# Kernel optimization log

Measured on AMD Instinct MI355X. Metric: run time of the kernel, lower is better.

Reference implementation:

```python
import jax, jax.numpy as jnp
import numpy as np

NUM_HEADS = 4


def setup_inputs() -> dict:
    key = jax.random.key(0)
    ks = jax.random.split(key, 5)
    B, S, E = 32, 1024, 512
    T, Q = 128, 256
    src_encodings = jax.random.normal(ks[0], (B, S, E), dtype=jnp.float32)
    src_token_mask = jax.random.randint(ks[1], (B, S), 0, 2).astype(bool)
    query_vec = jax.random.normal(ks[2], (T, B, Q), dtype=jnp.float32)
    # torch Linear weights are (out_features, in_features)
    W_src = jax.random.normal(ks[3], (NUM_HEADS * Q, E), dtype=jnp.float32) * (1.0 / np.sqrt(E))
    W_opt = jax.random.normal(ks[4], (NUM_HEADS, Q), dtype=jnp.float32) * (1.0 / np.sqrt(Q))
    return {"src_encodings": src_encodings, "src_token_mask": src_token_mask,
            "query_vec": query_vec, "W_src": W_src, "W_opt": W_opt}


def reference(src_encodings, src_token_mask, query_vec, W_src, W_opt):
    B, S, _ = src_encodings.shape
    T = query_vec.shape[0]
    Q = query_vec.shape[2]
    # project + leaky_relu (torch default negative_slope=0.01), split into heads
    proj = jax.nn.leaky_relu(jnp.einsum('bse,fe->bsf', src_encodings, W_src))  # (B,S,H*Q)
    proj = proj.reshape(B, S, NUM_HEADS, Q)                                    # (B,S,H,Q)
    # per-head scores: (T,B,S,H)
    weights = jnp.einsum('bshq,tbq->tbsh', proj, query_vec)
    # head routing: argmax over options scores (T,B,H) -> top-1 head per (t,b)
    options_scores = jnp.einsum('tbq,hq->tbh', query_vec, W_opt)
    best = jnp.argmax(options_scores, axis=-1)                                 # (T,B)
    w = jnp.take_along_axis(weights, best[:, :, None, None], axis=-1)[..., 0]  # (T,B,S)
    # mask and softmax over source positions
    w = jnp.where(src_token_mask[None, :, :], -jnp.inf, w)
    return jax.nn.softmax(w, axis=-1)
```

## Files before the change

### kernel.cpp

```cpp
#include <hip/hip_runtime.h>
#include <hip/hip_bf16.h>
#include <math.h>

#define B_ 32
#define S_ 1024
#define E_ 512
#define T_ 128
#define Q_ 256
#define H_ 4
#define F_ (H_ * Q_)
#define M_ (B_ * S_)

typedef _Float16 f16x8 __attribute__((ext_vector_type(8)));
typedef float f32x4 __attribute__((ext_vector_type(4)));
typedef unsigned int uint32;

__device__ __forceinline__ float lrelu(float x) { return x > 0.0f ? x : 0.01f * x; }

__device__ __forceinline__ uint32 packh2(float a, float b) {
    union { _Float16 h[2]; uint32 u; } v;
    v.h[0] = (_Float16)a; v.h[1] = (_Float16)b;
    return v.u;
}
__device__ __forceinline__ unsigned short packh1(float a) {
    union { _Float16 h; unsigned short u; } v;
    v.h = (_Float16)a;
    return v.u;
}

#define GLOAD_LDS16(g, l)                                                       \
    __builtin_amdgcn_global_load_lds(                                           \
        (const __attribute__((address_space(1))) void*)(g),                     \
        (__attribute__((address_space(3))) void*)(l), 16, 0, 0)

#define SRCW_BLOCKS 4096
#define WW_BLOCKS   128
#define HS_BLOCKS   1024

__global__ __launch_bounds__(256) void prep_kernel(
    float* src, float* wsrc,
    const float* __restrict__ qv, const float* __restrict__ Wopt,
    int* __restrict__ best) {
    const int blk = blockIdx.x;
    if (blk < SRCW_BLOCKS + WW_BLOCKS) {
        float* base = (blk < SRCW_BLOCKS) ? src : wsrc;
        const size_t w0 = (size_t)((blk < SRCW_BLOCKS) ? blk : (blk - SRCW_BLOCKS)) * 64;
        const int tid = threadIdx.x;
        const size_t c = w0 + (tid >> 2);
        const int j = tid & 3;
        const float* rp = base + c * 64 + j * 16;
        float4 v0 = ((const float4*)rp)[0];
        float4 v1 = ((const float4*)rp)[1];
        float4 v2 = ((const float4*)rp)[2];
        float4 v3 = ((const float4*)rp)[3];
        uint4 o0 = make_uint4(packh2(v0.x, v0.y), packh2(v0.z, v0.w),
                              packh2(v1.x, v1.y), packh2(v1.z, v1.w));
        uint4 o1 = make_uint4(packh2(v2.x, v2.y), packh2(v2.z, v2.w),
                              packh2(v3.x, v3.y), packh2(v3.z, v3.w));
        char* op = (char*)(base + c * 64) + j * 32;
        ((uint4*)op)[0] = o0;
        ((uint4*)op)[1] = o1;
    } else {
        const int wave = threadIdx.x >> 6, lane = threadIdx.x & 63;
        const int idx = (blk - SRCW_BLOCKS - WW_BLOCKS) * 4 + wave;
        const float4 qq = *(const float4*)(qv + (size_t)idx * Q_ + lane * 4);
        float s[4];
#pragma unroll
        for (int h = 0; h < 4; ++h) {
            float4 w = *(const float4*)(Wopt + h * Q_ + lane * 4);
            s[h] = qq.x * w.x + qq.y * w.y + qq.z * w.z + qq.w * w.w;
        }
#pragma unroll
        for (int off = 32; off >= 1; off >>= 1) {
#pragma unroll
            for (int h = 0; h < 4; ++h) s[h] += __shfl_down(s[h], off);
        }
        if (lane == 0) {
            int bh = 0; float bs = s[0];
            if (s[1] > bs) { bs = s[1]; bh = 1; }
            if (s[2] > bs) { bs = s[2]; bh = 2; }
            if (s[3] > bs) { bs = s[3]; bh = 3; }
            best[idx] = bh;
        }
    }
}

__global__ __launch_bounds__(256, 2) void proj_score_kernel(
    const unsigned char* __restrict__ Apk,
    const unsigned char* __restrict__ Wpk,
    const float* __restrict__ qv,
    const int* __restrict__ best,
    float* __restrict__ bufs)
{
    __shared__ uint4 smem4[4800];
    char* smem = (char*)smem4;

    const int bid = blockIdx.x;
    const int xcd = bid & 7;
    const int q_ = bid >> 3;
    const int bi = xcd * 32 + (q_ >> 2);
    const int bj = q_ & 3;

    const int tid = threadIdx.x;
    const int wave = tid >> 6, lane = tid & 63;
    const int wm = wave >> 1, wn = wave & 1;
    const int quad = lane >> 4;
    const int fr = lane & 15;
    const int xr = fr & 7;

    const size_t Abase = (size_t)(bi * 128) * 2048;
    const size_t Wbase = (size_t)(bj * 256) * 2048;

    const int r16 = lane >> 2;
    const int slot = lane & 3;
    const int sgb = ((slot ^ ((r16 >> 1) & 3)) & 3) * 16;
    const unsigned char* gA = Apk + Abase + (size_t)(wave * 32 + r16) * 2048 + sgb;
    const unsigned char* gW = Wpk + Wbase + (size_t)(wave * 64 + r16) * 2048 + sgb;

    const int koB = ((quad ^ ((fr >> 1) & 3)) & 3) * 16;
    const int aoff = (wm * 64 + fr) * 64 + koB;
    const int boff = (wn * 128 + fr) * 64 + koB;

    f32x4 acc[4][8] = {};

#define STAGE(bufb_, ks_) do {                                                 \
    const int hb_ = ((ks_) >> 1) * 256 + ((ks_) & 1) * 64;                     \
    _Pragma("unroll")                                                          \
    for (int c_ = 0; c_ < 2; ++c_) {                                           \
        GLOAD_LDS16(gA + (size_t)c_ * 16 * 2048 + hb_,                         \
                    smem + (bufb_) + (wave * 2 + c_) * 1024);                  \
    }                                                                          \
    _Pragma("unroll")                                                          \
    for (int c_ = 0; c_ < 4; ++c_) {                                           \
        GLOAD_LDS16(gW + (size_t)c_ * 16 * 2048 + hb_,                         \
                    smem + (bufb_) + 8192 + (wave * 4 + c_) * 1024);           \
    }                                                                          \
} while (0)

    STAGE(0, 0);
    STAGE(24576, 1);
    asm volatile("s_waitcnt vmcnt(6)" ::: "memory");
    __builtin_amdgcn_s_barrier();

    int cur = 0;
#pragma unroll 1
    for (int ks = 0; ks < 16; ++ks) {
        f16x8 ah[4], bh8[8];
#pragma unroll
        for (int i_ = 0; i_ < 4; ++i_)
            ah[i_] = *(const f16x8*)(smem + cur + aoff + i_ * 1024);
#pragma unroll
        for (int j_ = 0; j_ < 8; ++j_)
            bh8[j_] = *(const f16x8*)(smem + cur + 8192 + boff + j_ * 1024);
        asm volatile("s_waitcnt lgkmcnt(0)" ::: "memory");
        __builtin_amdgcn_s_barrier();
        if (ks < 14) STAGE(cur, ks + 2);
        __builtin_amdgcn_s_setprio(1);
#pragma unroll
        for (int i_ = 0; i_ < 4; ++i_)
#pragma unroll
            for (int j_ = 0; j_ < 8; ++j_) {
                acc[i_][j_] = __builtin_amdgcn_mfma_f32_16x16x32_f16(ah[i_], bh8[j_], acc[i_][j_], 0, 0, 0);
            }
        __builtin_amdgcn_s_setprio(0);
        if (ks < 14) {
            asm volatile("s_waitcnt vmcnt(6)" ::: "memory");
        } else if (ks == 14) {
            asm volatile("s_waitcnt vmcnt(0)" ::: "memory");
        }
        if (ks < 15) __builtin_amdgcn_s_barrier();
        cur ^= 24576;
    }

#undef STAGE

    const int b = bi >> 3;
    const int sbase = (bi & 7) * 128;

    __syncthreads();
    int* tl = (int*)(smem + 73728);
    int* lcnt = (int*)(smem + 74240);
    if (tid == 0) *lcnt = 0;
    __syncthreads();
    if (tid < 128) {
        if (best[tid * B_ + b] == bj) {
            int slot2 = atomicAdd(lcnt, 1);
            tl[slot2] = tid;
        }
    }
    __syncthreads();
    const int n = *lcnt;

#pragma unroll
    for (int i = 0; i < 4; ++i) {
#pragma unroll
        for (int j = 0; j < 8; ++j) {
            int col = wn * 128 + j * 16 + fr;
            int g = col >> 3;
            int cb = (col & 7) * 2;
#pragma unroll
            for (int r = 0; r < 4; ++r) {
                int rr = wm * 64 + i * 16 + quad * 4 + r;
                int gs = (g & 24) | ((g ^ rr) & 7);
                *(unsigned short*)(smem + rr * 512 + gs * 16 + cb) =
                    packh1(lrelu(acc[i][j][r]));
            }
        }
    }
    __syncthreads();

    const int t_idx = tid >> 4, seg = tid & 15;

    for (int tc = 0; tc < n; tc += 16) {
        int nn = min(16, n - tc);
        if (t_idx < nn) {
            int tt = tl[tc + t_idx];
            const float* qp = qv + ((size_t)tt * B_ + b) * Q_ + seg * 16;
            float4 f0 = *(const float4*)(qp);
            float4 f1 = *(const float4*)(qp + 4);
            float4 f2 = *(const float4*)(qp + 8);
            float4 f3 = *(const float4*)(qp + 12);
            uint4 h0 = make_uint4(packh2(f0.x, f0.y), packh2(f0.z, f0.w),
                                  packh2(f1.x, f1.y), packh2(f1.z, f1.w));
            uint4 h1 = make_uint4(packh2(f2.x, f2.y), packh2(f2.z, f2.w),
                                  packh2(f3.x, f3.y), packh2(f3.z, f3.w));
            int g0 = seg * 2, g1 = seg * 2 + 1;
            int gs0 = (g0 & 24) | ((g0 ^ t_idx) & 7);
            int gs1 = (g1 & 24) | ((g1 ^ t_idx) & 7);
            *(uint4*)(smem + 65536 + t_idx * 512 + gs0 * 16) = h0;
            *(uint4*)(smem + 65536 + t_idx * 512 + gs1 * 16) = h1;
        }
        __syncthreads();

#pragma unroll
        for (int sub = 0; sub < 2; ++sub) {
            const int sblk = wave * 2 + sub;
            const int srow = sblk * 16 + fr;
            f32x4 sc = {0.f, 0.f, 0.f, 0.f};
#pragma unroll
            for (int ks2 = 0; ks2 < 8; ++ks2) {
                int kb = ks2 * 4 + quad;
                int ko = ((kb & 24) | ((kb ^ xr) & 7)) * 16;
                f16x8 ph = *(const f16x8*)(smem + srow * 512 + ko);
                f16x8 qh = *(const f16x8*)(smem + 65536 + fr * 512 + ko);
                sc = __builtin_amdgcn_mfma_f32_16x16x32_f16(qh, ph, sc, 0, 0, 0);
            }
            int sg = sbase + sblk * 16 + fr;
#pragma unroll
            for (int r = 0; r < 4; ++r) {
                int tloc = quad * 4 + r;
                if (tloc < nn) {
                    int tg = tl[tc + tloc];
                    bufs[((size_t)tg * B_ + b) * S_ + sg] = sc[r];
                }
            }
        }
        __syncthreads();
    }
}

__global__ __launch_bounds__(256) void softmax_kernel(
    const float* __restrict__ bufs, float* __restrict__ out,
    const int* __restrict__ mask) {
    const int row = blockIdx.x;
    const int b = row & (B_ - 1);
    const float* w0 = bufs + (size_t)row * S_;
    float* w = out + (size_t)row * S_;
    const int* mrow = mask + (size_t)b * S_;
    const int tid = threadIdx.x;

    float4 va = *(const float4*)(w0 + tid * 4);
    int4 mm = *(const int4*)(mrow + tid * 4);
    float x0 = mm.x ? -INFINITY : va.x;
    float x1 = mm.y ? -INFINITY : va.y;
    float x2 = mm.z ? -INFINITY : va.z;
    float x3 = mm.w ? -INFINITY : va.w;

    float lmax = fmaxf(fmaxf(x0, x1), fmaxf(x2, x3));
#pragma unroll
    for (int off = 32; off >= 1; off >>= 1)
        lmax = fmaxf(lmax, __shfl_down(lmax, off));

    __shared__ float redmax[4];
    __shared__ float redsum[4];
    const int wave = tid >> 6, lane = tid & 63;
    if (lane == 0) redmax[wave] = lmax;
    __syncthreads();
    float gmax = fmaxf(fmaxf(redmax[0], redmax[1]), fmaxf(redmax[2], redmax[3]));

    float e0 = mm.x ? 0.f : __expf(x0 - gmax);
    float e1 = mm.y ? 0.f : __expf(x1 - gmax);
    float e2 = mm.z ? 0.f : __expf(x2 - gmax);
    float e3 = mm.w ? 0.f : __expf(x3 - gmax);
    float lsum = e0 + e1 + e2 + e3;
#pragma unroll
    for (int off = 32; off >= 1; off >>= 1)
        lsum += __shfl_down(lsum, off);
    if (lane == 0) redsum[wave] = lsum;
    __syncthreads();
    float gsum = redsum[0] + redsum[1] + redsum[2] + redsum[3];
    float rinv = 1.0f / gsum;

    *(float4*)(w + tid * 4) = make_float4(e0 * rinv, e1 * rinv, e2 * rinv, e3 * rinv);
}

extern "C" void kernel_launch(void* const* d_in, const int* in_sizes, int n_in,
                              void* d_out, int out_size, void* d_ws, size_t ws_size,
                              hipStream_t stream) {
    float* src  = (float*)d_in[0];
    const int* mask = (const int*)d_in[1];
    const float* qv = (const float*)d_in[2];
    float* Wsrc = (float*)d_in[3];
    const float* Wopt = (const float*)d_in[4];
    float* out = (float*)d_out;

    float* bufs = (float*)d_ws;
    int* best = (int*)((char*)d_ws + (size_t)T_ * B_ * S_ * sizeof(float));

    hipLaunchKernelGGL(prep_kernel, dim3(SRCW_BLOCKS + WW_BLOCKS + HS_BLOCKS), dim3(256),
                       0, stream, src, Wsrc, qv, Wopt, best);
    hipLaunchKernelGGL(proj_score_kernel, dim3(1024), dim3(256), 0, stream,
                       (const unsigned char*)src, (const unsigned char*)Wsrc,
                       qv, best, bufs);
    hipLaunchKernelGGL(softmax_kernel, dim3(T_ * B_), dim3(256), 0, stream,
                       bufs, out, mask);
}
```

Baseline: 165.8 us.

## Load A fragments directly from global into registers, stage only B in LDS

The A tile no longer goes through LDS. Each wave reads its own A fragments straight from global memory into registers, double-buffered across k-steps by unrolling the loop by two, while only the W/B tile is still staged in LDS through async global-to-LDS loads. This cuts LDS traffic and the LDS footprint per buffer. In exchange, the two waves that share a row block each load the same A data from global, and more vector registers are live. The vmcnt wait counts are adjusted to cover the extra outstanding A loads.

```diff
diff --git a/kernel.cpp b/kernel.cpp
--- a/kernel.cpp
+++ b/kernel.cpp
@@ -114,65 +114,71 @@
     const int r16 = lane >> 2;
     const int slot = lane & 3;
     const int sgb = ((slot ^ ((r16 >> 1) & 3)) & 3) * 16;
-    const unsigned char* gA = Apk + Abase + (size_t)(wave * 32 + r16) * 2048 + sgb;
     const unsigned char* gW = Wpk + Wbase + (size_t)(wave * 64 + r16) * 2048 + sgb;
 
+    const unsigned char* gAf = Apk + Abase + (size_t)(wm * 64 + fr) * 2048 + quad * 16;
+
     const int koB = ((quad ^ ((fr >> 1) & 3)) & 3) * 16;
-    const int aoff = (wm * 64 + fr) * 64 + koB;
     const int boff = (wn * 128 + fr) * 64 + koB;
 
     f32x4 acc[4][8] = {};
-
-#define STAGE(bufb_, ks_) do {                                                 \
+    f16x8 ah0[4], ah1[4];
+
+#define STAGE_B(bufb_, ks_) do {                                               \
     const int hb_ = ((ks_) >> 1) * 256 + ((ks_) & 1) * 64;                     \
-    _Pragma("unroll")                                                          \
-    for (int c_ = 0; c_ < 2; ++c_) {                                           \
-        GLOAD_LDS16(gA + (size_t)c_ * 16 * 2048 + hb_,                         \
-                    smem + (bufb_) + (wave * 2 + c_) * 1024);                  \
-    }                                                                          \
     _Pragma("unroll")                                                          \
     for (int c_ = 0; c_ < 4; ++c_) {                                           \
         GLOAD_LDS16(gW + (size_t)c_ * 16 * 2048 + hb_,                         \
-                    smem + (bufb_) + 8192 + (wave * 4 + c_) * 1024);           \
+                    smem + (bufb_) + (wave * 4 + c_) * 1024);                  \
     }                                                                          \
 } while (0)
 
-    STAGE(0, 0);
-    STAGE(24576, 1);
-    asm volatile("s_waitcnt vmcnt(6)" ::: "memory");
+#define LOADA(AH_, ks_) do {                                                   \
+    const int hb_ = ((ks_) >> 1) * 256 + ((ks_) & 1) * 64;                     \
+    _Pragma("unroll")                                                          \
+    for (int i_ = 0; i_ < 4; ++i_)                                             \
+        AH_[i_] = *(const f16x8*)(gAf + i_ * 32768 + hb_);                     \
+} while (0)
+
+#define KSTEP(AHc_, AHn_, ks_) do {                                            \
+    const int ksv_ = (ks_);                                                    \
+    f16x8 bh8[8];                                                              \
+    _Pragma("unroll")                                                          \
+    for (int j_ = 0; j_ < 8; ++j_)                                             \
+        bh8[j_] = *(const f16x8*)(smem + cur + boff + j_ * 1024);              \
+    asm volatile("s_waitcnt lgkmcnt(0)" ::: "memory");                         \
+    __builtin_amdgcn_s_barrier();                                              \
+    if (ksv_ <= 13) STAGE_B(cur, ksv_ + 2);                                    \
+    if (ksv_ <= 14) LOADA(AHn_, ksv_ + 1);                                     \
+    __builtin_amdgcn_s_setprio(1);                                             \
+    _Pragma("unroll")                                                          \
+    for (int i_ = 0; i_ < 4; ++i_)                                             \
+        _Pragma("unroll")                                                      \
+        for (int j_ = 0; j_ < 8; ++j_)                                         \
+            acc[i_][j_] = __builtin_amdgcn_mfma_f32_16x16x32_f16(AHc_[i_], bh8[j_], acc[i_][j_], 0, 0, 0); \
+    __builtin_amdgcn_s_setprio(0);                                             \
+    if (ksv_ <= 13) { asm volatile("s_waitcnt vmcnt(8)" ::: "memory"); }       \
+    else if (ksv_ == 14) { asm volatile("s_waitcnt vmcnt(4)" ::: "memory"); }  \
+    if (ksv_ <= 14) __builtin_amdgcn_s_barrier();                              \
+    cur ^= 16384;                                                              \
+} while (0)
+
+    STAGE_B(0, 0);
+    STAGE_B(16384, 1);
+    LOADA(ah0, 0);
+    asm volatile("s_waitcnt vmcnt(8)" ::: "memory");
     __builtin_amdgcn_s_barrier();
 
     int cur = 0;
 #pragma unroll 1
-    for (int ks = 0; ks < 16; ++ks) {
-        f16x8 ah[4], bh8[8];
-#pragma unroll
-        for (int i_ = 0; i_ < 4; ++i_)
-            ah[i_] = *(const f16x8*)(smem + cur + aoff + i_ * 1024);
-#pragma unroll
-        for (int j_ = 0; j_ < 8; ++j_)
-            bh8[j_] = *(const f16x8*)(smem + cur + 8192 + boff + j_ * 1024);
-        asm volatile("s_waitcnt lgkmcnt(0)" ::: "memory");
-        __builtin_amdgcn_s_barrier();
-        if (ks < 14) STAGE(cur, ks + 2);
-        __builtin_amdgcn_s_setprio(1);
-#pragma unroll
-        for (int i_ = 0; i_ < 4; ++i_)
-#pragma unroll
-            for (int j_ = 0; j_ < 8; ++j_) {
-                acc[i_][j_] = __builtin_amdgcn_mfma_f32_16x16x32_f16(ah[i_], bh8[j_], acc[i_][j_], 0, 0, 0);
-            }
-        __builtin_amdgcn_s_setprio(0);
-        if (ks < 14) {
-            asm volatile("s_waitcnt vmcnt(6)" ::: "memory");
-        } else if (ks == 14) {
-            asm volatile("s_waitcnt vmcnt(0)" ::: "memory");
-        }
-        if (ks < 15) __builtin_amdgcn_s_barrier();
-        cur ^= 24576;
-    }
-
-#undef STAGE
+    for (int kp = 0; kp < 8; ++kp) {
+        KSTEP(ah0, ah1, 2 * kp);
+        KSTEP(ah1, ah0, 2 * kp + 1);
+    }
+
+#undef STAGE_B
+#undef LOADA
+#undef KSTEP
 
     const int b = bi >> 3;
     const int sbase = (bi & 7) * 128;
```

Result: slower. 174.2 us (+5.1%).
